# Optimization experiments

Measured on AMD Instinct MI355X. Metric: run time of the kernel, lower is better.

## Reference

```python
import jax, jax.numpy as jnp
import numpy as np

N, M, F, W = 600000, 300000, 128, 256  # points, masked points, grid feat_dim, net width


def _lin_init(k, fi, fo):
    k1, k2 = jax.random.split(k)
    s = 1.0 / np.sqrt(fi)
    return (jax.random.uniform(k1, (fi, fo), jnp.float32, -s, s),
            jax.random.uniform(k2, (fo,), jnp.float32, -s, s))


def setup_inputs() -> dict:
    key = jax.random.key(0)
    ks = jax.random.split(key, 24)
    # unique sorted indices emulate the boolean target_mask (static count M)
    idx = jnp.asarray(np.sort(np.random.RandomState(0).permutation(N)[:M]).astype(np.int32))
    inp = {
        "rays_pts_emb": jax.random.normal(ks[0], (N, 3), jnp.float32),
        "rotations_emb": jax.random.normal(ks[1], (N, 4), jnp.float32),
        "shs_emb": jax.random.normal(ks[2], (N, 16, 3), jnp.float32),
        "time_emb": jax.random.uniform(ks[3], (N, 1), jnp.float32),
        "h_emb": jax.random.uniform(ks[4], (N, 1), jnp.float32),
        "grid_sp": jax.random.normal(ks[5], (M, F), jnp.float32),
        "grid_st": jax.random.normal(ks[6], (M, F), jnp.float32),
        "idx": idx,
    }
    layers = [("sp", F, W), ("st", F, W), ("p1", W, W), ("p2", W, 9),
              ("r1", W, W), ("r2", W, 4), ("s1", W, W), ("s2", W, 48),
              ("w1", W, W), ("w2", W, 1), ("m1", W, W), ("m2", W, 1)]
    for i, (nm, fi, fo) in enumerate(layers):
        Wt, b = _lin_init(ks[7 + i], fi, fo)
        inp["W_" + nm] = Wt
        inp["b_" + nm] = b
    return inp


def _head(x, W1, b1, W2, b2):
    # nn.Sequential(ReLU, Linear, ReLU, Linear)
    h = jax.nn.relu(x)
    h = jax.nn.relu(h @ W1 + b1)
    return h @ W2 + b2


def reference(rays_pts_emb, rotations_emb, shs_emb, time_emb, h_emb, grid_sp, grid_st, idx,
              W_sp, b_sp, W_st, b_st, W_p1, b_p1, W_p2, b_p2, W_r1, b_r1, W_r2, b_r2,
              W_s1, b_s1, W_s2, b_s2, W_w1, b_w1, W_w2, b_w2, W_m1, b_m1, W_m2, b_m2):
    # encoders (Linear only, no activation)
    sp = grid_sp @ W_sp + b_sp            # [M, W]
    st = grid_st @ W_st + b_st            # [M, W]
    t = time_emb[0:1]                     # [1, 1]
    mint = 1.0 - t
    # position deformation: Bezier combination of 3 control offsets
    dx = _head(sp, W_p1, b_p1, W_p2, b_p2).reshape(-1, 3, 3)  # [M, 3, 3]
    delta = (3.0 * mint ** 2 * t * dx[:, 0]
             + 3.0 * mint * t ** 2 * dx[:, 1]
             + t ** 3 * dx[:, 2])                              # [M, 3]
    pts = rays_pts_emb.at[idx].add(delta)
    rotations = rotations_emb.at[idx].add(_head(st, W_r1, b_r1, W_r2, b_r2))
    shs = shs_emb.at[idx].add(_head(st, W_s1, b_s1, W_s2, b_s2).reshape(-1, 16, 3))
    # opacity gating
    w = _head(sp, W_w1, b_w1, W_w2, b_w2) ** 2                 # [M, 1]
    mu = jax.nn.sigmoid(_head(sp, W_m1, b_m1, W_m2, b_m2))     # [M, 1]
    opacity = h_emb.at[idx].set(h_emb[idx] * jnp.exp(-w * (t - mu) ** 2))
    return (pts, rotations, opacity, shs)
```

## Files before the change

kernel.cpp:

```cpp
#include <hip/hip_runtime.h>
#include <hip/hip_bf16.h>
#include <stdint.h>

#define M_ROWS 300000

typedef __attribute__((ext_vector_type(8)))  short bf16x8;
typedef __attribute__((ext_vector_type(16))) float f32x16;
typedef __attribute__((ext_vector_type(4)))  float f32x4;

union U4 { uint4 u; bf16x8 h; unsigned short us[8]; };

__device__ __forceinline__ unsigned short f2bf(float f) {
  union { float f; uint32_t u; } v; v.f = f;
  uint32_t r = v.u + 0x7fffu + ((v.u >> 16) & 1u);
  return (unsigned short)(r >> 16);
}
__device__ __forceinline__ uint32_t pk2(float lo, float hi) {
  return (uint32_t)f2bf(lo) | ((uint32_t)f2bf(hi) << 16);
}
__device__ __forceinline__ f32x4 ntload4(const float* p) {
  return __builtin_nontemporal_load((const f32x4*)p);
}
__device__ __forceinline__ void ntstore4(float* p, f32x4 v) {
  __builtin_nontemporal_store(v, (f32x4*)p);
}

#define T_SP 0
#define T_ST 64
#define T_P1 128
#define T_P2 256
#define T_R1 272
#define T_R2 400
#define T_S1 416
#define T_S2 544
#define T_W1 576
#define T_W2 704
#define T_M1 720
#define T_M2 848
#define T_TOT 864

__global__ void prep_w(const float* Wsp, const float* Wst, const float* Wp1, const float* Wp2,
                       const float* Wr1, const float* Wr2, const float* Ws1, const float* Ws2,
                       const float* Ww1, const float* Ww2, const float* Wm1, const float* Wm2,
                       uint4* ws) {
  int b = blockIdx.x, l = threadIdx.x;
  const int starts[12] = {T_SP,T_ST,T_P1,T_P2,T_R1,T_R2,T_S1,T_S2,T_W1,T_W2,T_M1,T_M2};
  const int Ks[12]     = {128,128,256,256,256,256,256,256,256,256,256,256};
  const int Cos[12]    = {256,256,256,9,256,4,256,48,256,1,256,1};
  const float* Wp[12]  = {Wsp,Wst,Wp1,Wp2,Wr1,Wr2,Ws1,Ws2,Ww1,Ww2,Wm1,Wm2};
  int m = 0;
  #pragma unroll
  for (int i = 1; i < 12; ++i) if (b >= starts[i]) m = i;
  int local = b - starts[m];
  int KT = Ks[m] >> 4;
  int n0 = local / KT, k0 = local - n0 * KT;
  int col = n0 * 32 + (l & 31);
  int kbase = k0 * 16 + (l >> 5) * 8;
  const float* W = Wp[m];
  int Co = Cos[m];
  U4 pk;
  #pragma unroll
  for (int j = 0; j < 8; ++j) {
    float v = (col < Co) ? W[(size_t)(kbase + j) * Co + col] : 0.0f;
    pk.us[j] = f2bf(v);
  }
  ws[(size_t)b * 64 + l] = pk.u;
}

__global__ void copy_emb(const float* pts, const float* rot, const float* h,
                         const float* shs, float* out) {
  long long stride = (long long)gridDim.x * blockDim.x;
  for (long long i = (long long)blockIdx.x * blockDim.x + threadIdx.x; i < 8400000LL; i += stride) {
    if (i < 450000) {
      ntstore4(out + i * 4, ntload4(pts + i * 4));
    } else if (i < 1050000) {
      f32x4 v = ntload4(rot + (i - 450000) * 4);
      *(f32x4*)(out + i * 4) = v;
    } else if (i < 1200000) {
      ntstore4(out + i * 4, ntload4(h + (i - 1050000) * 4));
    } else {
      f32x4 v = ntload4(shs + (i - 1200000) * 4);
      *(f32x4*)(out + i * 4) = v;
    }
  }
}

#define LSTR 512
__device__ __forceinline__ int lds_addr(int row, int cb) {
  return row * LSTR + (cb ^ ((row & 15) << 4));
}

__device__ __forceinline__ void loadX(const float* grid, int row0, int t, char* buf) {
  #pragma unroll
  for (int i = 0; i < 2; ++i) {
    int fi = i * 512 + t;
    int row = fi >> 5;
    int c4 = fi & 31;
    f32x4 v = ntload4(grid + (size_t)(row0 + row) * 128 + c4 * 4);
    ushort4 p;
    p.x = f2bf(v.x); p.y = f2bf(v.y); p.z = f2bf(v.z); p.w = f2bf(v.w);
    *(ushort4*)(buf + lds_addr(row, c4 * 8)) = p;
  }
}

__device__ __forceinline__ void pre8(U4 (&d)[8], const uint4* base, int lane) {
  #pragma unroll
  for (int i = 0; i < 8; ++i) d[i].u = base[(size_t)i * 64 + lane];
}
__device__ __forceinline__ void pre4(U4 (&d)[8], const uint4* base, int lane) {
  #pragma unroll
  for (int i = 0; i < 4; ++i) d[i].u = base[(size_t)i * 64 + lane];
}
__device__ __forceinline__ void pre2(U4 (&d)[8], const uint4* base, int lane) {
  d[0].u = base[lane]; d[1].u = base[64 + lane];
}
__device__ __forceinline__ void pre_s2(U4 (&d)[8], const uint4* wt, int ct2, int kqs, int lane) {
  #pragma unroll
  for (int kk = 0; kk < 4; ++kk)
    d[kk].u = wt[(size_t)((ct2 * 16 + kqs * 4 + kk) * 64) + lane];
}

__device__ __forceinline__ void mm_big8S(U4 (&b)[8], const char* inb, int k0, int arow, int khalf,
                                         f32x16& acc) {
  #pragma unroll
  for (int k = 0; k < 8; ++k) {
    bf16x8 x = *(const bf16x8*)(inb + lds_addr(arow, (k0 + k) * 32 + khalf));
    acc = __builtin_amdgcn_mfma_f32_32x32x16_bf16(b[k].h, x, acc, 0, 0, 0);
  }
}

__device__ __forceinline__ void store_actS(char* outb, const float* bias, int wave, int lane,
                                           const f32x16& acc) {
  const int xr = lane & 31;
  const int cb0 = wave * 32 + 4 * (lane >> 5);
  #pragma unroll
  for (int run = 0; run < 4; ++run) {
    const int c0 = cb0 + 8 * run;
    const float4 bv = *(const float4*)(bias + c0);
    uint2 w;
    w.x = pk2(fmaxf(acc[run * 4 + 0] + bv.x, 0.0f), fmaxf(acc[run * 4 + 1] + bv.y, 0.0f));
    w.y = pk2(fmaxf(acc[run * 4 + 2] + bv.z, 0.0f), fmaxf(acc[run * 4 + 3] + bv.w, 0.0f));
    *(uint2*)(outb + lds_addr(xr, c0 * 2)) = w;
  }
}

__device__ __forceinline__ void mm_head2t(U4 (&b)[8], const char* inb, int kq8, int khalf,
                                          int lane, f32x16& acc) {
  const int arow = lane & 31;
  bf16x8 a0 = *(const bf16x8*)(inb + lds_addr(arow, (kq8 * 2 + 0) * 32 + khalf));
  bf16x8 a1 = *(const bf16x8*)(inb + lds_addr(arow, (kq8 * 2 + 1) * 32 + khalf));
  acc = __builtin_amdgcn_mfma_f32_32x32x16_bf16(a0, b[0].h, acc, 0, 0, 0);
  acc = __builtin_amdgcn_mfma_f32_32x32x16_bf16(a1, b[1].h, acc, 0, 0, 0);
}

template<int COLS>
__device__ __forceinline__ void head_atomic(float* outsm, int lane, const f32x16& acc) {
  int col = lane & 31;
  if (col < COLS) {
    #pragma unroll
    for (int q = 0; q < 16; ++q) {
      int row = (q & 3) + 8 * (q >> 2) + 4 * (lane >> 5);
      atomicAdd(&outsm[row * COLS + col], acc[q]);
    }
  }
}

__device__ __forceinline__ void rot_atomic_global(const f32x16& acc, int kq4, int lane,
                                                  const int* sidx, const float* b_r2,
                                                  float* out) {
  int col = lane & 31;
  if (col < 4) {
    float bb = (kq4 == 0) ? b_r2[col] : 0.0f;
    #pragma unroll
    for (int q = 0; q < 16; ++q) {
      int row = (q & 3) + 8 * (q >> 2) + 4 * (lane >> 5);
      atomicAdd(out + 1800000 + (size_t)sidx[row] * 4 + col, acc[q] + bb);
    }
  }
}

__device__ __forceinline__ void shs_atomic_global(const f32x16& acc, int ct2, int kqs, int lane,
                                                  const int* sidx, const float* b_s2,
                                                  float* out) {
  int c = lane & 31;
  int col = ct2 * 32 + c;
  if (col < 48) {
    float bb = (kqs == 0) ? b_s2[col] : 0.0f;
    #pragma unroll
    for (int q = 0; q < 16; ++q) {
      int row = (q & 3) + 8 * (q >> 2) + 4 * (lane >> 5);
      atomicAdd(out + 4800000 + (size_t)sidx[row] * 48 + col, acc[q] + bb);
    }
  }
}

__global__ void __launch_bounds__(512, 4) deform_main(
    const float* grid_sp, const float* grid_st, const int* idx,
    const float* rays, const float* rotq, const float* shs_in,
    const float* time_emb, const float* h_emb,
    const uint4* ws,
    const float* b_sp, const float* b_st, const float* b_p1, const float* b_p2,
    const float* b_r1, const float* b_r2, const float* b_s1, const float* b_s2,
    const float* b_w1, const float* b_w2, const float* b_m1, const float* b_m2,
    float* out) {
  __shared__ char bufA[16384];
  __shared__ char bufB[16384];
  __shared__ float smf[352];
  __shared__ int sidx[32];
  float* dxb = smf;
  float* wb  = smf + 288;
  float* mub = smf + 320;

  const int t = threadIdx.x;
  const int lane = t & 63;
  const int wave = t >> 6;
  const int kq8 = wave;
  const int kq4 = wave & 3;
  const int ct2 = wave & 1;
  const int kqs = wave >> 1;
  const int arow = lane & 31;
  const int khalf = (lane >> 5) * 16;
  const int row0 = blockIdx.x * 32;
  const float tt = time_emb[0];

  U4 b0[8], b1[8];
  pre8(b0, ws + (size_t)(T_SP + wave * 8) * 64, lane);

  if (t < 32) sidx[t] = idx[row0 + t];
  if (t < 352) smf[t] = 0.0f;
  loadX(grid_sp, row0, t, bufA);
  __syncthreads();

  {
    f32x16 acc = (f32x16)0.0f;
    pre8(b1, ws + (size_t)(T_P1 + wave * 16) * 64, lane);
    __builtin_amdgcn_s_setprio(1);
    mm_big8S(b0, bufA, 0, arow, khalf, acc);
    __builtin_amdgcn_s_setprio(0);
    store_actS(bufB, b_sp, wave, lane, acc);
  }
  __syncthreads();

  {
    f32x16 acc = (f32x16)0.0f;
    pre8(b0, ws + (size_t)(T_P1 + wave * 16 + 8) * 64, lane);
    __builtin_amdgcn_s_setprio(1);
    mm_big8S(b1, bufB, 0, arow, khalf, acc);
    __builtin_amdgcn_s_setprio(0);
    pre2(b1, ws + (size_t)(T_P2 + kq8 * 2) * 64, lane);
    __builtin_amdgcn_s_setprio(1);
    mm_big8S(b0, bufB, 8, arow, khalf, acc);
    __builtin_amdgcn_s_setprio(0);
    store_actS(bufA, b_p1, wave, lane, acc);
  }
  __syncthreads();

  {
    f32x16 hacc = (f32x16)0.0f;
    pre8(b0, ws + (size_t)(T_W1 + wave * 16) * 64, lane);
    __builtin_amdgcn_s_setprio(1);
    mm_head2t(b1, bufA, kq8, khalf, lane, hacc);
    __builtin_amdgcn_s_setprio(0);
    head_atomic<9>(dxb, lane, hacc);
  }
  __syncthreads();

  {
    f32x16 acc = (f32x16)0.0f;
    pre8(b1, ws + (size_t)(T_W1 + wave * 16 + 8) * 64, lane);
    __builtin_amdgcn_s_setprio(1);
    mm_big8S(b0, bufB, 0, arow, khalf, acc);
    __builtin_amdgcn_s_setprio(0);
    pre2(b0, ws + (size_t)(T_W2 + kq8 * 2) * 64, lane);
    __builtin_amdgcn_s_setprio(1);
    mm_big8S(b1, bufB, 8, arow, khalf, acc);
    __builtin_amdgcn_s_setprio(0);
    store_actS(bufA, b_w1, wave, lane, acc);
  }
  __syncthreads();

  {
    f32x16 hacc = (f32x16)0.0f;
    pre8(b1, ws + (size_t)(T_M1 + wave * 16) * 64, lane);
    __builtin_amdgcn_s_setprio(1);
    mm_head2t(b0, bufA, kq8, khalf, lane, hacc);
    __builtin_amdgcn_s_setprio(0);
    head_atomic<1>(wb, lane, hacc);
  }
  __syncthreads();

  {
    f32x16 acc = (f32x16)0.0f;
    pre8(b0, ws + (size_t)(T_M1 + wave * 16 + 8) * 64, lane);
    __builtin_amdgcn_s_setprio(1);
    mm_big8S(b1, bufB, 0, arow, khalf, acc);
    __builtin_amdgcn_s_setprio(0);
    pre2(b1, ws + (size_t)(T_M2 + kq8 * 2) * 64, lane);
    __builtin_amdgcn_s_setprio(1);
    mm_big8S(b0, bufB, 8, arow, khalf, acc);
    __builtin_amdgcn_s_setprio(0);
    store_actS(bufA, b_m1, wave, lane, acc);
  }
  __syncthreads();

  float pr = 0.0f, hv = 0.0f;
  {
    if (t < 128) {
      int row = t >> 2, sub = t & 3;
      int g = sidx[row];
      if (sub < 3) pr = rays[(size_t)g * 3 + sub]; else hv = h_emb[g];
    }
    loadX(grid_st, row0, t, bufB);
    f32x16 hacc = (f32x16)0.0f;
    __builtin_amdgcn_s_setprio(1);
    mm_head2t(b1, bufA, kq8, khalf, lane, hacc);
    __builtin_amdgcn_s_setprio(0);
    pre8(b0, ws + (size_t)(T_ST + wave * 8) * 64, lane);
    head_atomic<1>(mub, lane, hacc);
  }
  __syncthreads();

  {
    f32x16 acc = (f32x16)0.0f;
    pre8(b1, ws + (size_t)(T_R1 + wave * 16) * 64, lane);
    __builtin_amdgcn_s_setprio(1);
    mm_big8S(b0, bufB, 0, arow, khalf, acc);
    __builtin_amdgcn_s_setprio(0);
    store_actS(bufA, b_st, wave, lane, acc);
    if (t < 128) {
      int row = t >> 2, sub = t & 3;
      int g = sidx[row];
      if (sub < 3) {
        float mt = 1.0f - tt;
        float c0 = 3.0f * mt * mt * tt, c1 = 3.0f * mt * tt * tt, c2 = tt * tt * tt;
        float d0 = dxb[row * 9 + sub]     + b_p2[sub];
        float d1 = dxb[row * 9 + 3 + sub] + b_p2[3 + sub];
        float d2 = dxb[row * 9 + 6 + sub] + b_p2[6 + sub];
        __builtin_nontemporal_store(pr + (c0 * d0 + c1 * d1 + c2 * d2),
                                    out + (size_t)g * 3 + sub);
      } else {
        float wr = wb[row] + b_w2[0];
        float mr = mub[row] + b_m2[0];
        float mu = 1.0f / (1.0f + expf(-mr));
        float dtm = tt - mu;
        __builtin_nontemporal_store(hv * expf(-(wr * wr) * dtm * dtm),
                                    out + 4200000 + (size_t)g);
      }
    }
  }
  __syncthreads();

  {
    f32x16 acc = (f32x16)0.0f;
    pre8(b0, ws + (size_t)(T_R1 + wave * 16 + 8) * 64, lane);
    __builtin_amdgcn_s_setprio(1);
    mm_big8S(b1, bufA, 0, arow, khalf, acc);
    __builtin_amdgcn_s_setprio(0);
    pre4(b1, ws + (size_t)(T_R2 + kq4 * 4) * 64, lane);
    __builtin_amdgcn_s_setprio(1);
    mm_big8S(b0, bufA, 8, arow, khalf, acc);
    __builtin_amdgcn_s_setprio(0);
    store_actS(bufB, b_r1, wave, lane, acc);
  }
  __syncthreads();

  {
    if (wave < 4) {
      f32x16 hacc = (f32x16)0.0f;
      const int ar = lane & 31;
      __builtin_amdgcn_s_setprio(1);
      #pragma unroll
      for (int kk = 0; kk < 4; ++kk) {
        bf16x8 a = *(const bf16x8*)(bufB + lds_addr(ar, (kq4 * 4 + kk) * 32 + khalf));
        hacc = __builtin_amdgcn_mfma_f32_32x32x16_bf16(a, b1[kk].h, hacc, 0, 0, 0);
      }
      __builtin_amdgcn_s_setprio(0);
      rot_atomic_global(hacc, kq4, lane, sidx, b_r2, out);
    }
    pre8(b0, ws + (size_t)(T_S1 + wave * 16) * 64, lane);
  }
  __syncthreads();

  {
    f32x16 acc = (f32x16)0.0f;
    pre8(b1, ws + (size_t)(T_S1 + wave * 16 + 8) * 64, lane);
    __builtin_amdgcn_s_setprio(1);
    mm_big8S(b0, bufA, 0, arow, khalf, acc);
    __builtin_amdgcn_s_setprio(0);
    pre_s2(b0, ws + (size_t)T_S2 * 64, ct2, kqs, lane);
    __builtin_amdgcn_s_setprio(1);
    mm_big8S(b1, bufA, 8, arow, khalf, acc);
    __builtin_amdgcn_s_setprio(0);
    store_actS(bufB, b_s1, wave, lane, acc);
  }
  __syncthreads();

  {
    f32x16 hacc = (f32x16)0.0f;
    const int ar = lane & 31;
    __builtin_amdgcn_s_setprio(1);
    #pragma unroll
    for (int kk = 0; kk < 4; ++kk) {
      bf16x8 a = *(const bf16x8*)(bufB + lds_addr(ar, (kqs * 4 + kk) * 32 + khalf));
      hacc = __builtin_amdgcn_mfma_f32_32x32x16_bf16(a, b0[kk].h, hacc, 0, 0, 0);
    }
    __builtin_amdgcn_s_setprio(0);
    shs_atomic_global(hacc, ct2, kqs, lane, sidx, b_s2, out);
  }
}

extern "C" void kernel_launch(void* const* d_in, const int* in_sizes, int n_in,
                              void* d_out, int out_size, void* d_ws, size_t ws_size,
                              hipStream_t stream) {
  const float* rays     = (const float*)d_in[0];
  const float* rotq     = (const float*)d_in[1];
  const float* shs      = (const float*)d_in[2];
  const float* time_emb = (const float*)d_in[3];
  const float* h_emb    = (const float*)d_in[4];
  const float* grid_sp  = (const float*)d_in[5];
  const float* grid_st  = (const float*)d_in[6];
  const int*   idx      = (const int*)d_in[7];
  uint4* ws = (uint4*)d_ws;

  prep_w<<<T_TOT, 64, 0, stream>>>(
      (const float*)d_in[8],  (const float*)d_in[10], (const float*)d_in[12], (const float*)d_in[14],
      (const float*)d_in[16], (const float*)d_in[18], (const float*)d_in[20], (const float*)d_in[22],
      (const float*)d_in[24], (const float*)d_in[26], (const float*)d_in[28], (const float*)d_in[30],
      ws);

  copy_emb<<<2048, 256, 0, stream>>>(rays, rotq, h_emb, shs, (float*)d_out);

  deform_main<<<M_ROWS / 32, 512, 0, stream>>>(
      grid_sp, grid_st, idx, rays, rotq, shs, time_emb, h_emb, ws,
      (const float*)d_in[9],  (const float*)d_in[11], (const float*)d_in[13], (const float*)d_in[15],
      (const float*)d_in[17], (const float*)d_in[19], (const float*)d_in[21], (const float*)d_in[23],
      (const float*)d_in[25], (const float*)d_in[27], (const float*)d_in[29], (const float*)d_in[31],
      (float*)d_out);
}
```

Measured before the change: 664.3 us.

## Accumulate Bezier position deltas directly into global output via atomics

The position head partial sums are now scaled by their Bezier coefficients and atomically added straight into the global pts output, which already holds the copied rays. This removes the shared dx buffer, the later gather of rays, and the per-row combine step. The pts copy also switches to a regular store so the atomics can hit in cache. The LDS swizzle is widened to XOR with 5 row bits. In exchange it issues many more global atomics, which relies on the copy kernel finishing before the atomics run.

Result: slower. 1.174 ms (+76.8%).

```diff
diff --git a/kernel.cpp b/kernel.cpp
--- a/kernel.cpp
+++ b/kernel.cpp
@@ -72,7 +72,8 @@
   long long stride = (long long)gridDim.x * blockDim.x;
   for (long long i = (long long)blockIdx.x * blockDim.x + threadIdx.x; i < 8400000LL; i += stride) {
     if (i < 450000) {
-      ntstore4(out + i * 4, ntload4(pts + i * 4));
+      f32x4 v = ntload4(pts + i * 4);
+      *(f32x4*)(out + i * 4) = v;
     } else if (i < 1050000) {
       f32x4 v = ntload4(rot + (i - 450000) * 4);
       *(f32x4*)(out + i * 4) = v;
@@ -87,7 +88,7 @@
 
 #define LSTR 512
 __device__ __forceinline__ int lds_addr(int row, int cb) {
-  return row * LSTR + (cb ^ ((row & 15) << 4));
+  return row * LSTR + (cb ^ ((row & 31) << 4));
 }
 
 __device__ __forceinline__ void loadX(const float* grid, int row0, int t, char* buf) {
@@ -161,6 +162,24 @@
     for (int q = 0; q < 16; ++q) {
       int row = (q & 3) + 8 * (q >> 2) + 4 * (lane >> 5);
       atomicAdd(&outsm[row * COLS + col], acc[q]);
+    }
+  }
+}
+
+__device__ __forceinline__ void dx_atomic_global(const f32x16& hacc, int kq8, int lane,
+                                                 const int* sidx, const float* b_p2, float tt,
+                                                 float* out) {
+  int col = lane & 31;
+  if (col < 9) {
+    int comp = col % 3;
+    int seg = col / 3;
+    float mt = 1.0f - tt;
+    float coef = (seg == 0) ? 3.0f * mt * mt * tt : (seg == 1 ? 3.0f * mt * tt * tt : tt * tt * tt);
+    float bb = (kq8 == 0) ? coef * b_p2[col] : 0.0f;
+    #pragma unroll
+    for (int q = 0; q < 16; ++q) {
+      int row = (q & 3) + 8 * (q >> 2) + 4 * (lane >> 5);
+      atomicAdd(out + (size_t)sidx[row] * 3 + comp, coef * hacc[q] + bb);
     }
   }
 }
@@ -205,11 +224,10 @@
     float* out) {
   __shared__ char bufA[16384];
   __shared__ char bufB[16384];
-  __shared__ float smf[352];
+  __shared__ float smf[64];
   __shared__ int sidx[32];
-  float* dxb = smf;
-  float* wb  = smf + 288;
-  float* mub = smf + 320;
+  float* wb  = smf;
+  float* mub = smf + 32;
 
   const int t = threadIdx.x;
   const int lane = t & 63;
@@ -227,7 +245,7 @@
   pre8(b0, ws + (size_t)(T_SP + wave * 8) * 64, lane);
 
   if (t < 32) sidx[t] = idx[row0 + t];
-  if (t < 352) smf[t] = 0.0f;
+  if (t < 64) smf[t] = 0.0f;
   loadX(grid_sp, row0, t, bufA);
   __syncthreads();
 
@@ -261,7 +279,7 @@
     __builtin_amdgcn_s_setprio(1);
     mm_head2t(b1, bufA, kq8, khalf, lane, hacc);
     __builtin_amdgcn_s_setprio(0);
-    head_atomic<9>(dxb, lane, hacc);
+    dx_atomic_global(hacc, kq8, lane, sidx, b_p2, tt, out);
   }
   __syncthreads();
 
@@ -303,13 +321,9 @@
   }
   __syncthreads();
 
-  float pr = 0.0f, hv = 0.0f;
-  {
-    if (t < 128) {
-      int row = t >> 2, sub = t & 3;
-      int g = sidx[row];
-      if (sub < 3) pr = rays[(size_t)g * 3 + sub]; else hv = h_emb[g];
-    }
+  float hv = 0.0f;
+  {
+    if (t < 32) hv = h_emb[sidx[t]];
     loadX(grid_st, row0, t, bufB);
     f32x16 hacc = (f32x16)0.0f;
     __builtin_amdgcn_s_setprio(1);
@@ -327,25 +341,13 @@
     mm_big8S(b0, bufB, 0, arow, khalf, acc);
     __builtin_amdgcn_s_setprio(0);
     store_actS(bufA, b_st, wave, lane, acc);
-    if (t < 128) {
-      int row = t >> 2, sub = t & 3;
-      int g = sidx[row];
-      if (sub < 3) {
-        float mt = 1.0f - tt;
-        float c0 = 3.0f * mt * mt * tt, c1 = 3.0f * mt * tt * tt, c2 = tt * tt * tt;
-        float d0 = dxb[row * 9 + sub]     + b_p2[sub];
-        float d1 = dxb[row * 9 + 3 + sub] + b_p2[3 + sub];
-        float d2 = dxb[row * 9 + 6 + sub] + b_p2[6 + sub];
-        __builtin_nontemporal_store(pr + (c0 * d0 + c1 * d1 + c2 * d2),
-                                    out + (size_t)g * 3 + sub);
-      } else {
-        float wr = wb[row] + b_w2[0];
-        float mr = mub[row] + b_m2[0];
-        float mu = 1.0f / (1.0f + expf(-mr));
-        float dtm = tt - mu;
-        __builtin_nontemporal_store(hv * expf(-(wr * wr) * dtm * dtm),
-                                    out + 4200000 + (size_t)g);
-      }
+    if (t < 32) {
+      float wr = wb[t] + b_w2[0];
+      float mr = mub[t] + b_m2[0];
+      float mu = 1.0f / (1.0f + expf(-mr));
+      float dtm = tt - mu;
+      __builtin_nontemporal_store(hv * expf(-(wr * wr) * dtm * dtm),
+                                  out + 4200000 + (size_t)sidx[t]);
     }
   }
   __syncthreads();
```
